# Kernel tuning notes

Measured on AMD Instinct MI355X. Metric: run time of the kernel, lower is better.

Reference implementation:

```python
import jax, jax.numpy as jnp
import numpy as np
from jax.scipy.special import logsumexp

BS, SEQ, DM = 4, 4096, 1024
H, HD = 16, 64
BLK = 128
NB = SEQ // BLK          # 32 blocks
MAX_NB = 32
N_ITERS = 5
TEMP = 1.0
CLIP = 1.0


def setup_inputs() -> dict:
    key = jax.random.key(0)
    ks = jax.random.split(key, 12)
    s = 0.02
    return {
        'inputs_q': jax.random.normal(ks[0], (BS, SEQ, DM), jnp.float32),
        'wq': jax.random.normal(ks[1], (DM, H, HD), jnp.float32) * s,
        'bq': jnp.zeros((H, HD), jnp.float32),
        'wk': jax.random.normal(ks[2], (DM, H, HD), jnp.float32) * s,
        'bk': jnp.zeros((H, HD), jnp.float32),
        'wv': jax.random.normal(ks[3], (DM, H, HD), jnp.float32) * s,
        'bv': jnp.zeros((H, HD), jnp.float32),
        'w_sort': jax.random.normal(ks[4], (H, HD, MAX_NB), jnp.float32) * s,
        'b_sort': jnp.zeros((MAX_NB,), jnp.float32),
        'wo': jax.random.normal(ks[5], (H, HD, DM), jnp.float32) * s,
        'bo': jnp.zeros((DM,), jnp.float32),
    }


def sinkhorn_operator(log_alpha, n_iters=N_ITERS, temp=TEMP, clip=CLIP):
    # non-causal path of the original: iterative row/col log-normalization
    n = log_alpha.shape[1]
    la = jnp.reshape(log_alpha, (-1, n, n)) / temp
    for _ in range(n_iters):
        la = la - logsumexp(la, axis=2, keepdims=True)  # row normalize
        la = la - logsumexp(la, axis=1, keepdims=True)  # col normalize
    return jnp.exp(jnp.clip(la, -clip, clip))


def reference(inputs_q, wq, bq, wk, bk, wv, bv, w_sort, b_sort, wo, bo):
    bs, qlen, _ = inputs_q.shape
    nb = qlen // BLK
    # QKV projections: (bs, seq, H, HD)
    q = jnp.einsum('bsf,fhd->bshd', inputs_q, wq) + bq
    k = jnp.einsum('bsf,fhd->bshd', inputs_q, wk) + bk  # self-attention: inputs_kv = inputs_q
    v = jnp.einsum('bsf,fhd->bshd', inputs_q, wv) + bv
    # block reshape: (bs, nb, BLK, H, HD)
    qb = q.reshape(bs, nb, BLK, H, HD)
    kb = k.reshape(bs, nb, BLK, H, HD)
    vb = v.reshape(bs, nb, BLK, H, HD)
    # sort network: pool keys within block, project (H,HD)->MAX_NB
    sum_key = jnp.sum(kb, axis=2)                                   # (bs, nb, H, HD)
    sort_out = jnp.einsum('bnhd,hdm->bnm', sum_key, w_sort) + b_sort
    sort_mat = sort_out[:, :, :nb]                                  # (bs, nb, nb)
    perm = sinkhorn_operator(sort_mat)                              # (bs, nb, nb)
    # soft block sorting of keys/values
    sorted_k = jnp.einsum('bnm,bmshd->bnshd', perm, kb)
    sorted_v = jnp.einsum('bnm,bmshd->bnshd', perm, vb)
    # attend within each block to [local kv ; sorted kv]
    kcat = jnp.concatenate([kb, sorted_k], axis=2)                  # (bs, nb, 2BLK, H, HD)
    vcat = jnp.concatenate([vb, sorted_v], axis=2)
    scale = 1.0 / jnp.sqrt(jnp.float32(HD))
    logits = jnp.einsum('bnqhd,bnkhd->bnhqk', qb * scale, kcat)     # (bs, nb, H, BLK, 2BLK)
    w = jax.nn.softmax(logits, axis=-1)
    x = jnp.einsum('bnhqk,bnkhd->bnqhd', w, vcat)                   # (bs, nb, BLK, H, HD)
    x = x.reshape(bs, qlen, H, HD)
    return jnp.einsum('bshd,hdf->bsf', x, wo) + bo
```

## Files before the change

### kernel.cpp

```cpp
#include <hip/hip_runtime.h>
#include <stdint.h>

typedef short bf16x8 __attribute__((ext_vector_type(8)));
typedef float f32x4 __attribute__((ext_vector_type(4)));
typedef unsigned short u16;
typedef unsigned short u16x4 __attribute__((ext_vector_type(4)));

#define AS1 __attribute__((address_space(1)))
#define AS3 __attribute__((address_space(3)))

__device__ __forceinline__ void gll16(const void* g, void* l) {
  __builtin_amdgcn_global_load_lds((const AS1 uint32_t*)g, (AS3 uint32_t*)l, 16, 0, 0);
}

__device__ __forceinline__ f32x4 mfma16(bf16x8 a, bf16x8 b, f32x4 c) {
  return __builtin_amdgcn_mfma_f32_16x16x32_bf16(a, b, c, 0, 0, 0);
}

__device__ __forceinline__ u16 f2bf(float f) {
  union { float f; uint32_t u; } c; c.f = f;
  uint32_t r = c.u + 0x7FFFu + ((c.u >> 16) & 1u);
  return (u16)(r >> 16);
}
__device__ __forceinline__ float bf2f(u16 h) {
  union { uint32_t u; float f; } c; c.u = ((uint32_t)h) << 16; return c.f;
}

__global__ __launch_bounds__(256) void k_cast(const float* __restrict__ in, u16* __restrict__ out) {
  int i = (blockIdx.x * 256 + threadIdx.x) * 4;
  float4 v = *(const float4*)(in + i);
  u16x4 r; r.x = f2bf(v.x); r.y = f2bf(v.y); r.z = f2bf(v.z); r.w = f2bf(v.w);
  *(u16x4*)(out + i) = r;
}

__global__ __launch_bounds__(1024) void k_transpose4(
    const float* __restrict__ wq, const float* __restrict__ wk,
    const float* __restrict__ wv, const float* __restrict__ wo,
    u16* __restrict__ Wqkvt, u16* __restrict__ Wot) {
  __shared__ float t[32][33];
  const float* src; u16* dst;
  int z = blockIdx.z;
  if (z == 0)      { src = wq; dst = Wqkvt; }
  else if (z == 1) { src = wk; dst = Wqkvt + 1024 * 1024; }
  else if (z == 2) { src = wv; dst = Wqkvt + 2 * 1024 * 1024; }
  else             { src = wo; dst = Wot; }
  int tx = threadIdx.x, ty = threadIdx.y;
  t[ty][tx] = src[(size_t)(blockIdx.y * 32 + ty) * 1024 + blockIdx.x * 32 + tx];
  __syncthreads();
  dst[(size_t)(blockIdx.x * 32 + ty) * 1024 + blockIdx.y * 32 + tx] = f2bf(t[tx][ty]);
}

__global__ __launch_bounds__(256, 4) void k_gemm_qkv(
    const u16* __restrict__ A, const u16* __restrict__ Bt,
    const float* __restrict__ bq, const float* __restrict__ bk, const float* __restrict__ bv,
    u16* __restrict__ Qb, u16* __restrict__ Kb, u16* __restrict__ Vbt, float* __restrict__ sumk)
{
  __shared__ u16 As[128 * 32];
  __shared__ u16 Bs[128 * 32];
  int tid = threadIdx.x, lane = tid & 63, w = tid >> 6;
  int wm = w >> 1, wn = w & 1;
  int m0 = blockIdx.y * 128, n0 = blockIdx.x * 128;

  int l4 = lane >> 2;
  int p = (lane & 3) ^ ((lane >> 3) & 3);
  const u16* Ag0 = A + (size_t)(m0 + w * 32 + l4) * 1024 + p * 8;
  const u16* Ag1 = A + (size_t)(m0 + w * 32 + 16 + l4) * 1024 + p * 8;
  const u16* Bg0 = Bt + (size_t)(n0 + w * 32 + l4) * 1024 + p * 8;
  const u16* Bg1 = Bt + (size_t)(n0 + w * 32 + 16 + l4) * 1024 + p * 8;
  u16* La0 = As + w * 1024; u16* La1 = As + w * 1024 + 512;
  u16* Lb0 = Bs + w * 1024; u16* Lb1 = Bs + w * 1024 + 512;

  int mm = lane & 15, quad = lane >> 4;
  int sw = quad ^ ((mm >> 1) & 3);
  const bf16x8* pa[4]; const bf16x8* pb[4];
#pragma unroll
  for (int t = 0; t < 4; ++t) {
    pa[t] = (const bf16x8*)(As + (wm * 64 + t * 16 + mm) * 32 + sw * 8);
    pb[t] = (const bf16x8*)(Bs + (wn * 64 + t * 16 + mm) * 32 + sw * 8);
  }

  f32x4 acc[4][4];
#pragma unroll
  for (int i = 0; i < 4; ++i)
#pragma unroll
    for (int j = 0; j < 4; ++j) acc[i][j] = (f32x4){0.f, 0.f, 0.f, 0.f};

  for (int kt = 0; kt < 32; ++kt) {
    int ko = kt * 32;
    gll16(Ag0 + ko, La0); gll16(Ag1 + ko, La1);
    gll16(Bg0 + ko, Lb0); gll16(Bg1 + ko, Lb1);
    __syncthreads();
    bf16x8 a[4], b[4];
#pragma unroll
    for (int t = 0; t < 4; ++t) { a[t] = *pa[t]; b[t] = *pb[t]; }
#pragma unroll
    for (int i = 0; i < 4; ++i)
#pragma unroll
      for (int j = 0; j < 4; ++j) acc[i][j] = mfma16(a[i], b[j], acc[i][j]);
    __syncthreads();
  }

  int sel = n0 >> 10;
  const float* bias = sel == 0 ? bq : (sel == 1 ? bk : bv);
  float scl = sel == 0 ? 0.125f : 1.0f;
#pragma unroll
  for (int j = 0; j < 4; ++j) {
    int ng = n0 + wn * 64 + j * 16 + mm;
    int h = (ng >> 6) & 15, d = ng & 63;
    float bval = bias[ng & 1023];
#pragma unroll
    for (int i = 0; i < 4; ++i)
#pragma unroll
      for (int r = 0; r < 4; ++r) {
        int mg = m0 + wm * 64 + i * 16 + quad * 4 + r;
        int b_ = mg >> 12, s = mg & 4095;
        float v = (acc[i][j][r] + bval) * scl;
        if (sel == 0)      Qb [((size_t)(b_ * 16 + h) * 4096 + s) * 64 + d] = f2bf(v);
        else if (sel == 1) Kb [((size_t)(b_ * 16 + h) * 4096 + s) * 64 + d] = f2bf(v);
        else               Vbt[((size_t)(b_ * 16 + h) * 64 + d) * 4096 + s] = f2bf(v);
      }
  }

  if (sel == 1) {
    float cs[4];
#pragma unroll
    for (int j = 0; j < 4; ++j) {
      int ng = n0 + wn * 64 + j * 16 + mm;
      float bval = bias[ng & 1023];
      float s = 16.f * bval;
#pragma unroll
      for (int i = 0; i < 4; ++i)
#pragma unroll
        for (int r = 0; r < 4; ++r) s += acc[i][j][r];
      s += __shfl_xor(s, 16);
      s += __shfl_xor(s, 32);
      cs[j] = s;
    }
    float* red = (float*)As;
    if (quad == 0) {
#pragma unroll
      for (int j = 0; j < 4; ++j) red[wm * 128 + wn * 64 + j * 16 + mm] = cs[j];
    }
    __syncthreads();
    if (tid < 128) {
      int b_ = m0 >> 12, n = (m0 >> 7) & 31;
      sumk[(size_t)(b_ * 32 + n) * 1024 + (n0 - 1024) + tid] = red[tid] + red[128 + tid];
    }
  }
}

__global__ __launch_bounds__(256, 4) void k_gemm_out(
    const u16* __restrict__ A, const u16* __restrict__ Bt,
    const float* __restrict__ bo, float* __restrict__ out)
{
  __shared__ u16 As[128 * 32];
  __shared__ u16 Bs[128 * 32];
  int tid = threadIdx.x, lane = tid & 63, w = tid >> 6;
  int wm = w >> 1, wn = w & 1;
  int m0 = blockIdx.y * 128, n0 = blockIdx.x * 128;
  int l4 = lane >> 2;
  int p = (lane & 3) ^ ((lane >> 3) & 3);
  const u16* Ag0 = A + (size_t)(m0 + w * 32 + l4) * 1024 + p * 8;
  const u16* Ag1 = A + (size_t)(m0 + w * 32 + 16 + l4) * 1024 + p * 8;
  const u16* Bg0 = Bt + (size_t)(n0 + w * 32 + l4) * 1024 + p * 8;
  const u16* Bg1 = Bt + (size_t)(n0 + w * 32 + 16 + l4) * 1024 + p * 8;
  u16* La0 = As + w * 1024; u16* La1 = As + w * 1024 + 512;
  u16* Lb0 = Bs + w * 1024; u16* Lb1 = Bs + w * 1024 + 512;
  int mm = lane & 15, quad = lane >> 4;
  int sw = quad ^ ((mm >> 1) & 3);
  const bf16x8* pa[4]; const bf16x8* pb[4];
#pragma unroll
  for (int t = 0; t < 4; ++t) {
    pa[t] = (const bf16x8*)(As + (wm * 64 + t * 16 + mm) * 32 + sw * 8);
    pb[t] = (const bf16x8*)(Bs + (wn * 64 + t * 16 + mm) * 32 + sw * 8);
  }
  f32x4 acc[4][4];
#pragma unroll
  for (int i = 0; i < 4; ++i)
#pragma unroll
    for (int j = 0; j < 4; ++j) acc[i][j] = (f32x4){0.f, 0.f, 0.f, 0.f};
  for (int kt = 0; kt < 32; ++kt) {
    int ko = kt * 32;
    gll16(Ag0 + ko, La0); gll16(Ag1 + ko, La1);
    gll16(Bg0 + ko, Lb0); gll16(Bg1 + ko, Lb1);
    __syncthreads();
    bf16x8 a[4], b[4];
#pragma unroll
    for (int t = 0; t < 4; ++t) { a[t] = *pa[t]; b[t] = *pb[t]; }
#pragma unroll
    for (int i = 0; i < 4; ++i)
#pragma unroll
      for (int j = 0; j < 4; ++j) acc[i][j] = mfma16(a[i], b[j], acc[i][j]);
    __syncthreads();
  }
#pragma unroll
  for (int j = 0; j < 4; ++j) {
    int ng = n0 + wn * 64 + j * 16 + mm;
    float bval = bo[ng];
#pragma unroll
    for (int i = 0; i < 4; ++i)
#pragma unroll
      for (int r = 0; r < 4; ++r) {
        int mg = m0 + wm * 64 + i * 16 + quad * 4 + r;
        out[(size_t)mg * 1024 + ng] = acc[i][j][r] + bval;
      }
  }
}

__global__ __launch_bounds__(256) void k_sortmm(const float* __restrict__ sumk, const float* __restrict__ wsort,
                                                const float* __restrict__ bsort, float* __restrict__ so) {
  __shared__ float red[256];
  int n = blockIdx.x, b = blockIdx.y, t = threadIdx.x;
  int m = t & 31, kp = t >> 5;
  const float* row = sumk + (size_t)(b * 32 + n) * 1024;
  float acc = 0.f;
  for (int c = kp * 128; c < kp * 128 + 128; ++c) acc += row[c] * wsort[c * 32 + m];
  red[t] = acc;
  __syncthreads();
  if (t < 32) {
    float s = bsort[t];
#pragma unroll
    for (int q = 0; q < 8; ++q) s += red[q * 32 + t];
    so[(size_t)(b * 32 + n) * 32 + t] = s;
  }
}

__global__ __launch_bounds__(32) void k_sinkhorn(const float* __restrict__ so, float* __restrict__ perm) {
  __shared__ float A[32][33];
  int b = blockIdx.x, t = threadIdx.x;
  for (int i = 0; i < 32; ++i) A[i][t] = so[(size_t)(b * 32 + i) * 32 + t];
  __syncthreads();
  for (int it = 0; it < 5; ++it) {
    {
      float mx = -1e30f;
      for (int j = 0; j < 32; ++j) mx = fmaxf(mx, A[t][j]);
      float s = 0.f;
      for (int j = 0; j < 32; ++j) s += __expf(A[t][j] - mx);
      float l = mx + __logf(s);
      for (int j = 0; j < 32; ++j) A[t][j] -= l;
    }
    __syncthreads();
    {
      float mx = -1e30f;
      for (int j = 0; j < 32; ++j) mx = fmaxf(mx, A[j][t]);
      float s = 0.f;
      for (int j = 0; j < 32; ++j) s += __expf(A[j][t] - mx);
      float l = mx + __logf(s);
      for (int j = 0; j < 32; ++j) A[j][t] -= l;
    }
    __syncthreads();
  }
  for (int i = 0; i < 32; ++i)
    perm[(size_t)(b * 32 + i) * 32 + t] = __expf(fminf(fmaxf(A[i][t], -1.f), 1.f));
}

__global__ __launch_bounds__(256) void k_mix(
    const u16* __restrict__ Kb, const u16* __restrict__ Vbt, const float* __restrict__ perm,
    u16* __restrict__ Ksort, u16* __restrict__ Vsort)
{
  __shared__ float P[32][32];
  int b = blockIdx.z, y = blockIdx.y, xg = blockIdx.x;
  int tid = threadIdx.x;
#pragma unroll
  for (int i = 0; i < 4; ++i) {
    int idx = i * 256 + tid;
    P[idx >> 5][idx & 31] = perm[b * 1024 + idx];
  }
  __syncthreads();
  if (y < 16) {
    int h = y;
    int ss = xg * 4 + (tid >> 6), d = tid & 63;
    const u16* Kg = Kb + (size_t)(b * 16 + h) * 262144;
    float xk[32];
#pragma unroll
    for (int m = 0; m < 32; ++m) xk[m] = bf2f(Kg[(size_t)(m * 128 + ss) * 64 + d]);
    size_t tbase = (size_t)((b * 16 + h) * 32) * 8192;
#pragma unroll
    for (int nn = 0; nn < 32; ++nn) {
      float sk = 0.f;
#pragma unroll
      for (int m4 = 0; m4 < 8; ++m4) {
        float4 pv = *(const float4*)&P[nn][m4 * 4];
        sk += pv.x * xk[m4 * 4 + 0] + pv.y * xk[m4 * 4 + 1] + pv.z * xk[m4 * 4 + 2] + pv.w * xk[m4 * 4 + 3];
      }
      Ksort[tbase + (size_t)nn * 8192 + ss * 64 + d] = f2bf(sk);
    }
  } else {
    int h = y - 16;
    int d = xg * 2 + (tid >> 7), ss = tid & 127;
    const u16* Vg = Vbt + ((size_t)(b * 16 + h) * 64 + d) * 4096;
    float xv[32];
#pragma unroll
    for (int m = 0; m < 32; ++m) xv[m] = bf2f(Vg[m * 128 + ss]);
    size_t tbase = (size_t)((b * 16 + h) * 32) * 8192;
#pragma unroll
    for (int nn = 0; nn < 32; ++nn) {
      float sv = 0.f;
#pragma unroll
      for (int m4 = 0; m4 < 8; ++m4) {
        float4 pv = *(const float4*)&P[nn][m4 * 4];
        sv += pv.x * xv[m4 * 4 + 0] + pv.y * xv[m4 * 4 + 1] + pv.z * xv[m4 * 4 + 2] + pv.w * xv[m4 * 4 + 3];
      }
      Vsort[tbase + (size_t)nn * 8192 + d * 128 + ss] = f2bf(sv);
    }
  }
}

__global__ __launch_bounds__(256, 2) void k_attn(
    const u16* __restrict__ Qb, const u16* __restrict__ Kb, const u16* __restrict__ Ksort,
    const u16* __restrict__ Vbt, const u16* __restrict__ Vsort, u16* __restrict__ X)
{
  __shared__ u16 Ks[16384];
  __shared__ u16 Vlo[8192];
  __shared__ u16 Vhi[8192];
  int tid = threadIdx.x, lane = tid & 63, w = tid >> 6;
  int n = blockIdx.x, h = blockIdx.y, b = blockIdx.z;
  size_t bh = (size_t)(b * 16 + h);
  size_t tileK = bh * 32 + n;

  {
    int l8 = lane >> 3, sl8 = lane & 7;
    const u16* Korig = Kb + (bh * 4096 + (size_t)n * 128) * 64;
    const u16* Ksrt  = Ksort + tileK * 8192;
#pragma unroll
    for (int c = 0; c < 8; ++c) {
      int cc = w * 8 + c;
      int r = cc * 8 + l8;
      int pk = sl8 ^ (r & 7);
      const u16* src = (cc < 16) ? (Korig + (size_t)r * 64 + pk * 8)
                                 : (Ksrt + (size_t)(r - 128) * 64 + pk * 8);
      gll16(src, Ks + cc * 512);
    }
    int l16 = lane >> 4, sl16 = lane & 15;
    const u16* Vorig = Vbt + bh * 262144 + (size_t)n * 128;
    const u16* Vsrt  = Vsort + tileK * 8192;
#pragma unroll
    for (int c = 0; c < 4; ++c) {
      int cc = w * 4 + c;
      int d = cc * 4 + l16;
      int pv = sl16 ^ (d & 15);
      gll16(Vorig + (size_t)d * 4096 + pv * 8, Vlo + cc * 512);
      gll16(Vsrt + (size_t)d * 128 + pv * 8, Vhi + cc * 512);
    }
  }

  int mm = lane & 15, quad = lane >> 4;
  bf16x8 qf[2][2];
  {
    size_t qrow = bh * 4096 + n * 128 + w * 32;
#pragma unroll
    for (int mt = 0; mt < 2; ++mt)
#pragma unroll
      for (int ks = 0; ks < 2; ++ks)
        qf[mt][ks] = *(const bf16x8*)(Qb + (qrow + mt * 16 + mm) * 64 + ks * 32 + quad * 8);
  }
  __syncthreads();

  f32x4 S[2][16];
#pragma unroll
  for (int mt = 0; mt < 2; ++mt)
#pragma unroll
    for (int nt = 0; nt < 16; ++nt) S[mt][nt] = (f32x4){0.f, 0.f, 0.f, 0.f};
#pragma unroll
  for (int nt = 0; nt < 16; ++nt) {
    int kk = nt * 16 + mm;
#pragma unroll
    for (int ks = 0; ks < 2; ++ks) {
      int ch = (ks * 4 + quad) ^ (kk & 7);
      bf16x8 bk = *(const bf16x8*)(Ks + kk * 64 + ch * 8);
      S[0][nt] = mfma16(qf[0][ks], bk, S[0][nt]);
      S[1][nt] = mfma16(qf[1][ks], bk, S[1][nt]);
    }
  }

  float mx[2][4], ls[2][4];
#pragma unroll
  for (int mt = 0; mt < 2; ++mt)
#pragma unroll
    for (int r = 0; r < 4; ++r) {
      float v = S[mt][0][r];
#pragma unroll
      for (int nt = 1; nt < 16; ++nt) v = fmaxf(v, S[mt][nt][r]);
#pragma unroll
      for (int o = 1; o < 16; o <<= 1) v = fmaxf(v, __shfl_xor(v, o));
      mx[mt][r] = v;
    }
#pragma unroll
  for (int mt = 0; mt < 2; ++mt)
#pragma unroll
    for (int nt = 0; nt < 16; ++nt)
#pragma unroll
      for (int r = 0; r < 4; ++r)
        S[mt][nt][r] = __expf(S[mt][nt][r] - mx[mt][r]);
#pragma unroll
  for (int mt = 0; mt < 2; ++mt)
#pragma unroll
    for (int r = 0; r < 4; ++r) {
      float s = 0.f;
#pragma unroll
      for (int nt = 0; nt < 16; ++nt) s += S[mt][nt][r];
#pragma unroll
      for (int o = 1; o < 16; o <<= 1) s += __shfl_xor(s, o);
      ls[mt][r] = s;
    }

  __syncthreads();

  u16* Pw = Ks + w * 4096;
  f32x4 O[2][4];
#pragma unroll
  for (int mt = 0; mt < 2; ++mt)
#pragma unroll
    for (int dt = 0; dt < 4; ++dt) O[mt][dt] = (f32x4){0.f, 0.f, 0.f, 0.f};

#pragma unroll
  for (int half = 0; half < 2; ++half) {
    const u16* Vp = half == 0 ? Vlo : Vhi;
#pragma unroll
    for (int mt = 0; mt < 2; ++mt)
#pragma unroll
      for (int nt8 = 0; nt8 < 8; ++nt8) {
        int nt = half * 8 + nt8;
        int kkl = nt8 * 16 + mm;
#pragma unroll
        for (int r = 0; r < 4; ++r) {
          int q = mt * 16 + quad * 4 + r;
          int ch = (kkl >> 3) ^ (q & 15);
          Pw[q * 128 + ch * 8 + (kkl & 7)] = f2bf(S[mt][nt][r]);
        }
      }
#pragma unroll
    for (int ksl = 0; ksl < 4; ++ksl) {
      bf16x8 pa[2];
#pragma unroll
      for (int mt = 0; mt < 2; ++mt) {
        int q = mt * 16 + mm;
        int ch = (ksl * 4 + quad) ^ (q & 15);
        pa[mt] = *(const bf16x8*)(Pw + q * 128 + ch * 8);
      }
#pragma unroll
      for (int dt = 0; dt < 4; ++dt) {
        int d = dt * 16 + mm;
        int ch = (ksl * 4 + quad) ^ (d & 15);
        bf16x8 vb = *(const bf16x8*)(Vp + d * 128 + ch * 8);
        O[0][dt] = mfma16(pa[0], vb, O[0][dt]);
        O[1][dt] = mfma16(pa[1], vb, O[1][dt]);
      }
    }
  }

#pragma unroll
  for (int mt = 0; mt < 2; ++mt)
#pragma unroll
    for (int dt = 0; dt < 4; ++dt)
#pragma unroll
      for (int r = 0; r < 4; ++r) {
        int q = w * 32 + mt * 16 + quad * 4 + r;
        float val = O[mt][dt][r] / ls[mt][r];
        size_t row = (size_t)b * 4096 + n * 128 + q;
        X[row * 1024 + h * 64 + dt * 16 + mm] = f2bf(val);
      }
}

extern "C" void kernel_launch(void* const* d_in, const int* in_sizes, int n_in,
                              void* d_out, int out_size, void* d_ws, size_t ws_size,
                              hipStream_t stream) {
  const float* inq   = (const float*)d_in[0];
  const float* wq    = (const float*)d_in[1];
  const float* bq    = (const float*)d_in[2];
  const float* wk    = (const float*)d_in[3];
  const float* bk    = (const float*)d_in[4];
  const float* wv    = (const float*)d_in[5];
  const float* bv    = (const float*)d_in[6];
  const float* wsort = (const float*)d_in[7];
  const float* bsort = (const float*)d_in[8];
  const float* wo    = (const float*)d_in[9];
  const float* bo    = (const float*)d_in[10];
  float* out = (float*)d_out;

  char* ws = (char*)d_ws;
  size_t off = 0;
  auto alloc = [&](size_t bytes) { char* p = ws + off; off += (bytes + 255) & ~(size_t)255; return p; };
  u16*  Qb    = (u16*)alloc(33554432);
  u16*  Kb    = (u16*)alloc(33554432);
  u16*  Vbt   = (u16*)alloc(33554432);
  u16*  Ksort = (u16*)alloc(33554432);
  u16*  Vsort = (u16*)alloc(33554432);
  u16*  Abf   = (u16*)alloc(33554432);
  u16*  Wqkvt = (u16*)alloc(6291456);
  u16*  Wot   = (u16*)alloc(2097152);
  float* sumk = (float*)alloc(524288);
  float* so   = (float*)alloc(16384);
  float* perm = (float*)alloc(16384);
  u16*  X = Abf;

  k_cast<<<16384, 256, 0, stream>>>(inq, Abf);
  k_transpose4<<<dim3(32, 32, 4), dim3(32, 32), 0, stream>>>(wq, wk, wv, wo, Wqkvt, Wot);
  k_gemm_qkv<<<dim3(24, 128), 256, 0, stream>>>(Abf, Wqkvt, bq, bk, bv, Qb, Kb, Vbt, sumk);
  k_sortmm<<<dim3(32, 4), 256, 0, stream>>>(sumk, wsort, bsort, so);
  k_sinkhorn<<<4, 32, 0, stream>>>(so, perm);
  k_mix<<<dim3(32, 32, 4), 256, 0, stream>>>(Kb, Vbt, perm, Ksort, Vsort);
  k_attn<<<dim3(32, 16, 4), 256, 0, stream>>>(Qb, Kb, Ksort, Vbt, Vsort, X);
  k_gemm_out<<<dim3(8, 128), 256, 0, stream>>>(X, Wot, bo, out);
}
```

Before: 495.6 us.

## Replace QKV and output GEMMs with 256x256 double-buffered pipelined MFMA mainloop

Both projection GEMMs now share a 256x256-tile, 8-wave mainloop with K-step 64. Global-to-LDS loads are double-buffered and interleaved with the MFMA phases, using explicit waitcnt, barriers and raised wave priority. This targets the per-step full syncs and small-tile reuse limits of the old 128x128, K=32 loop. In exchange it needs 128KB of LDS and more accumulator registers, and the grids shrink to 768 and 256 blocks, which risks occupancy and load-balance problems. The sumk reduction now writes one 128-row block per wave row directly, without an LDS reduction.

New measurement: 509.6 us. +2.8%, slower.

```diff
diff --git a/kernel.cpp b/kernel.cpp
--- a/kernel.cpp
+++ b/kernel.cpp
@@ -50,71 +50,134 @@
   dst[(size_t)(blockIdx.x * 32 + ty) * 1024 + blockIdx.y * 32 + tx] = f2bf(t[tx][ty]);
 }
 
-__global__ __launch_bounds__(256, 4) void k_gemm_qkv(
+__device__ __forceinline__ void gemm256_loop(
+    const u16* __restrict__ Ag, const u16* __restrict__ Bg,
+    u16* lds, int m0, int n0, f32x4 (&acc)[8][4])
+{
+  const int tid = threadIdx.x, lane = tid & 63, w = tid >> 6;
+  const int wm = w >> 2, wn = w & 3;
+  const int l8 = lane >> 3, c7 = lane & 7;
+  const int mm = lane & 15, quad = lane >> 4;
+  const int ch0 = (quad ^ (mm & 7)) * 8;
+  const int ch1 = ((quad ^ (mm & 7)) ^ 4) * 8;
+
+  const u16* aSt = Ag + (size_t)(m0 + w * 8 + l8) * 1024 + (c7 ^ l8) * 8;
+  const u16* bSt = Bg + (size_t)(n0 + w * 8 + l8) * 1024 + (c7 ^ l8) * 8;
+  u16* ldsAw = lds + w * 512;
+  u16* ldsBw = lds + 32768 + w * 512;
+  const u16* aR0 = lds + (wm * 128 + mm) * 64 + ch0;
+  const u16* aR1 = lds + (wm * 128 + mm) * 64 + ch1;
+  const u16* bR0 = lds + 32768 + (wn * 64 + mm) * 64 + ch0;
+  const u16* bR1 = lds + 32768 + (wn * 64 + mm) * 64 + ch1;
+
+#define STA(q, kt, buf) gll16(aSt + (q) * 65536 + (kt) * 64, ldsAw + (buf) * 16384 + (q) * 4096)
+#define STB(q, kt, buf) gll16(bSt + (q) * 65536 + (kt) * 64, ldsBw + (buf) * 16384 + (q) * 4096)
+
+#pragma unroll
+  for (int i = 0; i < 8; ++i)
+#pragma unroll
+    for (int j = 0; j < 4; ++j) acc[i][j] = (f32x4){0.f, 0.f, 0.f, 0.f};
+
+  STA(0, 0, 0); STA(1, 0, 0); STA(2, 0, 0); STA(3, 0, 0);
+  STB(0, 0, 0); STB(1, 0, 0); STB(2, 0, 0); STB(3, 0, 0);
+  STA(0, 1, 1); STA(2, 1, 1);
+  asm volatile("s_waitcnt vmcnt(2)" ::: "memory");
+  __builtin_amdgcn_s_barrier();
+
+#define PH(C, MH, NH, STAGE) do {                                                        \
+    bf16x8 af[4][2]; bf16x8 bf[2][2];                                                    \
+    _Pragma("unroll")                                                                    \
+    for (int i = 0; i < 4; ++i) {                                                        \
+      af[i][0] = *(const bf16x8*)(aR0 + (C) * 16384 + ((MH) * 64 + i * 16) * 64);        \
+      af[i][1] = *(const bf16x8*)(aR1 + (C) * 16384 + ((MH) * 64 + i * 16) * 64);        \
+    }                                                                                    \
+    _Pragma("unroll")                                                                    \
+    for (int j = 0; j < 2; ++j) {                                                        \
+      bf[j][0] = *(const bf16x8*)(bR0 + (C) * 16384 + ((NH) * 32 + j * 16) * 64);        \
+      bf[j][1] = *(const bf16x8*)(bR1 + (C) * 16384 + ((NH) * 32 + j * 16) * 64);        \
+    }                                                                                    \
+    STAGE                                                                                \
+    __builtin_amdgcn_s_barrier();                                                        \
+    asm volatile("s_waitcnt lgkmcnt(0)" ::: "memory");                                   \
+    __builtin_amdgcn_sched_barrier(0);                                                   \
+    __builtin_amdgcn_s_setprio(1);                                                       \
+    _Pragma("unroll")                                                                    \
+    for (int ks = 0; ks < 2; ++ks)                                                       \
+      _Pragma("unroll")                                                                  \
+      for (int i = 0; i < 4; ++i)                                                        \
+        _Pragma("unroll")                                                                \
+        for (int j = 0; j < 2; ++j)                                                      \
+          acc[(MH) * 4 + i][(NH) * 2 + j] =                                              \
+              mfma16(af[i][ks], bf[j][ks], acc[(MH) * 4 + i][(NH) * 2 + j]);             \
+    __builtin_amdgcn_s_setprio(0);                                                       \
+  } while (0)
+
+#pragma unroll 1
+  for (int t = 0; t < 16; t += 2) {
+    {
+      const int t1 = t + 1, t2 = t + 2;
+      const bool s2 = t2 < 16;
+      PH(0, 0, 0, { STA(1, t1, 1); STA(3, t1, 1); });
+      __builtin_amdgcn_s_barrier();
+      PH(0, 0, 1, { STB(0, t1, 1); STB(1, t1, 1); });
+      __builtin_amdgcn_s_barrier();
+      PH(0, 1, 0, { STB(2, t1, 1); STB(3, t1, 1); if (s2) { STA(0, t2, 0); STA(2, t2, 0); } });
+      __builtin_amdgcn_s_barrier();
+      PH(0, 1, 1, {});
+      if (s2) asm volatile("s_waitcnt vmcnt(2)" ::: "memory");
+      else    asm volatile("s_waitcnt vmcnt(0)" ::: "memory");
+      __builtin_amdgcn_s_barrier();
+    }
+    {
+      const int t2 = t + 2, t3 = t + 3;
+      const bool s1 = t2 < 16, s2 = t3 < 16;
+      PH(1, 0, 0, { if (s1) { STA(1, t2, 0); STA(3, t2, 0); } });
+      __builtin_amdgcn_s_barrier();
+      PH(1, 0, 1, { if (s1) { STB(0, t2, 0); STB(1, t2, 0); } });
+      __builtin_amdgcn_s_barrier();
+      PH(1, 1, 0, { if (s1) { STB(2, t2, 0); STB(3, t2, 0); } if (s2) { STA(0, t3, 1); STA(2, t3, 1); } });
+      __builtin_amdgcn_s_barrier();
+      PH(1, 1, 1, {});
+      if (s2)      asm volatile("s_waitcnt vmcnt(2)" ::: "memory");
+      else if (s1) asm volatile("s_waitcnt vmcnt(0)" ::: "memory");
+      __builtin_amdgcn_s_barrier();
+    }
+  }
+#undef PH
+#undef STA
+#undef STB
+}
+
+__global__ __launch_bounds__(512, 2) void k_gemm_qkv(
     const u16* __restrict__ A, const u16* __restrict__ Bt,
     const float* __restrict__ bq, const float* __restrict__ bk, const float* __restrict__ bv,
     u16* __restrict__ Qb, u16* __restrict__ Kb, u16* __restrict__ Vbt, float* __restrict__ sumk)
 {
-  __shared__ u16 As[128 * 32];
-  __shared__ u16 Bs[128 * 32];
-  int tid = threadIdx.x, lane = tid & 63, w = tid >> 6;
-  int wm = w >> 1, wn = w & 1;
-  int m0 = blockIdx.y * 128, n0 = blockIdx.x * 128;
-
-  int l4 = lane >> 2;
-  int p = (lane & 3) ^ ((lane >> 3) & 3);
-  const u16* Ag0 = A + (size_t)(m0 + w * 32 + l4) * 1024 + p * 8;
-  const u16* Ag1 = A + (size_t)(m0 + w * 32 + 16 + l4) * 1024 + p * 8;
-  const u16* Bg0 = Bt + (size_t)(n0 + w * 32 + l4) * 1024 + p * 8;
-  const u16* Bg1 = Bt + (size_t)(n0 + w * 32 + 16 + l4) * 1024 + p * 8;
-  u16* La0 = As + w * 1024; u16* La1 = As + w * 1024 + 512;
-  u16* Lb0 = Bs + w * 1024; u16* Lb1 = Bs + w * 1024 + 512;
-
-  int mm = lane & 15, quad = lane >> 4;
-  int sw = quad ^ ((mm >> 1) & 3);
-  const bf16x8* pa[4]; const bf16x8* pb[4];
-#pragma unroll
-  for (int t = 0; t < 4; ++t) {
-    pa[t] = (const bf16x8*)(As + (wm * 64 + t * 16 + mm) * 32 + sw * 8);
-    pb[t] = (const bf16x8*)(Bs + (wn * 64 + t * 16 + mm) * 32 + sw * 8);
-  }
-
-  f32x4 acc[4][4];
-#pragma unroll
-  for (int i = 0; i < 4; ++i)
-#pragma unroll
-    for (int j = 0; j < 4; ++j) acc[i][j] = (f32x4){0.f, 0.f, 0.f, 0.f};
-
-  for (int kt = 0; kt < 32; ++kt) {
-    int ko = kt * 32;
-    gll16(Ag0 + ko, La0); gll16(Ag1 + ko, La1);
-    gll16(Bg0 + ko, Lb0); gll16(Bg1 + ko, Lb1);
-    __syncthreads();
-    bf16x8 a[4], b[4];
-#pragma unroll
-    for (int t = 0; t < 4; ++t) { a[t] = *pa[t]; b[t] = *pb[t]; }
-#pragma unroll
-    for (int i = 0; i < 4; ++i)
-#pragma unroll
-      for (int j = 0; j < 4; ++j) acc[i][j] = mfma16(a[i], b[j], acc[i][j]);
-    __syncthreads();
-  }
-
-  int sel = n0 >> 10;
+  __shared__ __align__(16) u16 LDS[65536];
+  const int m0 = blockIdx.y * 256, n0 = blockIdx.x * 256;
+  f32x4 acc[8][4];
+  gemm256_loop(A, Bt, LDS, m0, n0, acc);
+
+  const int tid = threadIdx.x, lane = tid & 63, w = tid >> 6;
+  const int wm = w >> 2, wn = w & 3;
+  const int mm = lane & 15, quad = lane >> 4;
+  const int sel = n0 >> 10;
   const float* bias = sel == 0 ? bq : (sel == 1 ? bk : bv);
-  float scl = sel == 0 ? 0.125f : 1.0f;
-#pragma unroll
-  for (int j = 0; j < 4; ++j) {
-    int ng = n0 + wn * 64 + j * 16 + mm;
-    int h = (ng >> 6) & 15, d = ng & 63;
-    float bval = bias[ng & 1023];
-#pragma unroll
-    for (int i = 0; i < 4; ++i)
+  const float scl = sel == 0 ? 0.125f : 1.0f;
+
+#pragma unroll
+  for (int nf = 0; nf < 4; ++nf) {
+    int ngl = n0 + wn * 64 + nf * 16 + mm;
+    int nq = ngl & 1023;
+    int h = nq >> 6, d = nq & 63;
+    float bval = bias[nq];
+#pragma unroll
+    for (int mf = 0; mf < 8; ++mf)
 #pragma unroll
       for (int r = 0; r < 4; ++r) {
-        int mg = m0 + wm * 64 + i * 16 + quad * 4 + r;
+        int mg = m0 + wm * 128 + mf * 16 + quad * 4 + r;
         int b_ = mg >> 12, s = mg & 4095;
-        float v = (acc[i][j][r] + bval) * scl;
+        float v = (acc[mf][nf][r] + bval) * scl;
         if (sel == 0)      Qb [((size_t)(b_ * 16 + h) * 4096 + s) * 64 + d] = f2bf(v);
         else if (sel == 1) Kb [((size_t)(b_ * 16 + h) * 4096 + s) * 64 + d] = f2bf(v);
         else               Vbt[((size_t)(b_ * 16 + h) * 64 + d) * 4096 + s] = f2bf(v);
@@ -122,87 +185,46 @@
   }
 
   if (sel == 1) {
-    float cs[4];
-#pragma unroll
-    for (int j = 0; j < 4; ++j) {
-      int ng = n0 + wn * 64 + j * 16 + mm;
-      float bval = bias[ng & 1023];
-      float s = 16.f * bval;
-#pragma unroll
-      for (int i = 0; i < 4; ++i)
-#pragma unroll
-        for (int r = 0; r < 4; ++r) s += acc[i][j][r];
-      s += __shfl_xor(s, 16);
-      s += __shfl_xor(s, 32);
-      cs[j] = s;
-    }
-    float* red = (float*)As;
-    if (quad == 0) {
-#pragma unroll
-      for (int j = 0; j < 4; ++j) red[wm * 128 + wn * 64 + j * 16 + mm] = cs[j];
-    }
-    __syncthreads();
-    if (tid < 128) {
-      int b_ = m0 >> 12, n = (m0 >> 7) & 31;
-      sumk[(size_t)(b_ * 32 + n) * 1024 + (n0 - 1024) + tid] = red[tid] + red[128 + tid];
-    }
-  }
-}
-
-__global__ __launch_bounds__(256, 4) void k_gemm_out(
+#pragma unroll
+    for (int nf = 0; nf < 4; ++nf) {
+      float ssum = 0.f;
+#pragma unroll
+      for (int mf = 0; mf < 8; ++mf)
+#pragma unroll
+        for (int r = 0; r < 4; ++r) ssum += acc[mf][nf][r];
+      ssum += __shfl_xor(ssum, 16);
+      ssum += __shfl_xor(ssum, 32);
+      if (quad == 0) {
+        int colg = (n0 - 1024) + wn * 64 + nf * 16 + mm;
+        int b_ = m0 >> 12, nb2 = ((m0 >> 7) & 31) + wm;
+        sumk[(size_t)(b_ * 32 + nb2) * 1024 + colg] = ssum + 128.f * bias[colg];
+      }
+    }
+  }
+}
+
+__global__ __launch_bounds__(512, 2) void k_gemm_out(
     const u16* __restrict__ A, const u16* __restrict__ Bt,
     const float* __restrict__ bo, float* __restrict__ out)
 {
-  __shared__ u16 As[128 * 32];
-  __shared__ u16 Bs[128 * 32];
-  int tid = threadIdx.x, lane = tid & 63, w = tid >> 6;
-  int wm = w >> 1, wn = w & 1;
-  int m0 = blockIdx.y * 128, n0 = blockIdx.x * 128;
-  int l4 = lane >> 2;
-  int p = (lane & 3) ^ ((lane >> 3) & 3);
-  const u16* Ag0 = A + (size_t)(m0 + w * 32 + l4) * 1024 + p * 8;
-  const u16* Ag1 = A + (size_t)(m0 + w * 32 + 16 + l4) * 1024 + p * 8;
-  const u16* Bg0 = Bt + (size_t)(n0 + w * 32 + l4) * 1024 + p * 8;
-  const u16* Bg1 = Bt + (size_t)(n0 + w * 32 + 16 + l4) * 1024 + p * 8;
-  u16* La0 = As + w * 1024; u16* La1 = As + w * 1024 + 512;
-  u16* Lb0 = Bs + w * 1024; u16* Lb1 = Bs + w * 1024 + 512;
-  int mm = lane & 15, quad = lane >> 4;
-  int sw = quad ^ ((mm >> 1) & 3);
-  const bf16x8* pa[4]; const bf16x8* pb[4];
-#pragma unroll
-  for (int t = 0; t < 4; ++t) {
-    pa[t] = (const bf16x8*)(As + (wm * 64 + t * 16 + mm) * 32 + sw * 8);
-    pb[t] = (const bf16x8*)(Bs + (wn * 64 + t * 16 + mm) * 32 + sw * 8);
-  }
-  f32x4 acc[4][4];
-#pragma unroll
-  for (int i = 0; i < 4; ++i)
-#pragma unroll
-    for (int j = 0; j < 4; ++j) acc[i][j] = (f32x4){0.f, 0.f, 0.f, 0.f};
-  for (int kt = 0; kt < 32; ++kt) {
-    int ko = kt * 32;
-    gll16(Ag0 + ko, La0); gll16(Ag1 + ko, La1);
-    gll16(Bg0 + ko, Lb0); gll16(Bg1 + ko, Lb1);
-    __syncthreads();
-    bf16x8 a[4], b[4];
-#pragma unroll
-    for (int t = 0; t < 4; ++t) { a[t] = *pa[t]; b[t] = *pb[t]; }
-#pragma unroll
-    for (int i = 0; i < 4; ++i)
-#pragma unroll
-      for (int j = 0; j < 4; ++j) acc[i][j] = mfma16(a[i], b[j], acc[i][j]);
-    __syncthreads();
-  }
-#pragma unroll
-  for (int j = 0; j < 4; ++j) {
-    int ng = n0 + wn * 64 + j * 16 + mm;
+  __shared__ __align__(16) u16 LDS[65536];
+  const int m0 = blockIdx.y * 256, n0 = blockIdx.x * 256;
+  f32x4 acc[8][4];
+  gemm256_loop(A, Bt, LDS, m0, n0, acc);
+
+  const int tid = threadIdx.x, lane = tid & 63, w = tid >> 6;
+  const int wm = w >> 2, wn = w & 3;
+  const int mm = lane & 15, quad = lane >> 4;
+#pragma unroll
+  for (int nf = 0; nf < 4; ++nf) {
+    int ng = n0 + wn * 64 + nf * 16 + mm;
     float bval = bo[ng];
 #pragma unroll
-    for (int i = 0; i < 4; ++i)
+    for (int mf = 0; mf < 8; ++mf)
 #pragma unroll
       for (int r = 0; r < 4; ++r) {
-        int mg = m0 + wm * 64 + i * 16 + quad * 4 + r;
-        out[(size_t)mg * 1024 + ng] = acc[i][j][r] + bval;
+        int mg = m0 + wm * 128 + mf * 16 + quad * 4 + r;
+        out[(size_t)mg * 1024 + ng] = acc[mf][nf][r] + bval;
       }
   }
 }
@@ -496,10 +518,10 @@
 
   k_cast<<<16384, 256, 0, stream>>>(inq, Abf);
   k_transpose4<<<dim3(32, 32, 4), dim3(32, 32), 0, stream>>>(wq, wk, wv, wo, Wqkvt, Wot);
-  k_gemm_qkv<<<dim3(24, 128), 256, 0, stream>>>(Abf, Wqkvt, bq, bk, bv, Qb, Kb, Vbt, sumk);
+  k_gemm_qkv<<<dim3(12, 64), 512, 0, stream>>>(Abf, Wqkvt, bq, bk, bv, Qb, Kb, Vbt, sumk);
   k_sortmm<<<dim3(32, 4), 256, 0, stream>>>(sumk, wsort, bsort, so);
   k_sinkhorn<<<4, 32, 0, stream>>>(so, perm);
   k_mix<<<dim3(32, 32, 4), 256, 0, stream>>>(Kb, Vbt, perm, Ksort, Vsort);
   k_attn<<<dim3(32, 16, 4), 256, 0, stream>>>(Qb, Kb, Ksort, Vbt, Vsort, X);
-  k_gemm_out<<<dim3(8, 128), 256, 0, stream>>>(X, Wot, bo, out);
-}
+  k_gemm_out<<<dim3(4, 64), 512, 0, stream>>>(X, Wot, bo, out);
+}
```
